# Kernel optimization log

Hardware: AMD Instinct MI355X
Metric: run time of the kernel (lower is better)

## Reference

```python
import jax, jax.numpy as jnp
import numpy as np

N_NODES = 100000
N_EDGES = 3200000
FEAT = 32
N_ITER = 6  # -> n_iter - 1 = 5 SimpleConv layers
MIN_VAL, MAX_VAL = 0.0, 2.0


def setup_inputs() -> dict:
    key = jax.random.key(0)
    k = jax.random.split(key, 6)
    return {
        "x": jax.random.uniform(k[0], (N_NODES, FEAT), dtype=jnp.float32) * 2.0,
        "edge_index": jax.random.randint(k[1], (2, N_EDGES), 0, N_NODES, dtype=jnp.int32),
        "edge_mask": jax.random.randint(k[2], (N_EDGES,), 0, 2, dtype=jnp.int32),
        "edge_scale": jax.random.uniform(k[3], (N_EDGES,), dtype=jnp.float32),
        "pert_mask": jax.random.uniform(k[4], (N_EDGES,), dtype=jnp.float32),
        "edge_weight": jax.random.uniform(k[5], (N_EDGES,), dtype=jnp.float32),
    }


def reference(x, edge_index, edge_mask, edge_scale, pert_mask, edge_weight):
    # edge_index *= edge_mask (masked edges collapse to node 0, as in the torch code)
    ei = edge_index * edge_mask.astype(edge_index.dtype)  # [2, E]
    src, dst = ei[0], ei[1]
    # edge_weight = (edge_weight * (1 - pert_mask) + pert_mask) * edge_scale
    w = (edge_weight * (1.0 - pert_mask) + pert_mask) * edge_scale  # [E]

    def step(x, _):
        # SimpleConv(aggr='sum'): out[dst] += w_e * x[src]
        msgs = x[src] * w[:, None]                                   # [E, F]
        x_new = jax.ops.segment_sum(msgs, dst, num_segments=N_NODES)  # [N, F]
        # max_update: x + Hardtanh(-1,1)(x_new - x)
        x_new = x + jnp.clip(x_new - x, -1.0, 1.0)
        # act: Hardtanh(min_val, max_val)
        return jnp.clip(x_new, MIN_VAL, MAX_VAL), None

    x, _ = jax.lax.scan(step, x, None, length=N_ITER - 1)
    return x
```

## Files before the change

kernel.cpp:

```cpp
#include <hip/hip_runtime.h>
#include <hip/hip_fp16.h>

#define NNODES 100000
#define NEDGES 3200000
#define FEAT 32
#define NITER 5
#define NF (NNODES * FEAT)

#define EDGE_BLOCKS (NEDGES / 256)

#define BUCK_SH 8
#define BUCK_SZ 256
#define NBK 391
#define CHUNKF 4096
#define NBF 782
#define NT (NBF * NBK)
#define NTB 299

__global__ void ws_kernel(const int* __restrict__ edge_index,
                          const int* __restrict__ edge_mask,
                          const float* __restrict__ edge_scale,
                          const float* __restrict__ pert_mask,
                          const float* __restrict__ edge_weight,
                          int2* __restrict__ pay,
                          unsigned short* __restrict__ bkt,
                          float* __restrict__ S_part) {
    const int e = blockIdx.x * 256 + threadIdx.x;
    const int m = edge_mask[e];
    const float w = (edge_weight[e] * (1.0f - pert_mask[e]) + pert_mask[e]) * edge_scale[e];
    const int src = edge_index[e];
    const int dst = edge_index[NEDGES + e];
    pay[e] = make_int2(src | ((dst & (BUCK_SZ - 1)) << 20), __float_as_int(w));
    bkt[e] = m ? (unsigned short)(dst >> BUCK_SH) : (unsigned short)0xFFFFu;
    float ms = m ? 0.0f : w;
    __shared__ float s[256];
    s[threadIdx.x] = ms;
    __syncthreads();
    for (int off = 128; off; off >>= 1) {
        if (threadIdx.x < off) s[threadIdx.x] += s[threadIdx.x + off];
        __syncthreads();
    }
    if (threadIdx.x == 0) S_part[blockIdx.x] = s[0];
}

__global__ void sreduce_kernel(const float* __restrict__ S_part, float* __restrict__ S) {
    __shared__ float s[1024];
    float a = 0.0f;
    for (int i = threadIdx.x; i < EDGE_BLOCKS; i += 1024) a += S_part[i];
    s[threadIdx.x] = a;
    __syncthreads();
    for (int off = 512; off; off >>= 1) {
        if (threadIdx.x < off) s[threadIdx.x] += s[threadIdx.x + off];
        __syncthreads();
    }
    if (threadIdx.x == 0) *S = s[0];
}

__global__ void histmat_kernel(const unsigned short* __restrict__ bkt, int* __restrict__ M) {
    __shared__ int h[NBK];
    const int b = blockIdx.x;
    for (int k = threadIdx.x; k < NBK; k += 256) h[k] = 0;
    __syncthreads();
    const int base = b * CHUNKF;
    for (int it = 0; it < CHUNKF / 256; ++it) {
        const int e = base + it * 256 + threadIdx.x;
        if (e < NEDGES) {
            const unsigned short k = bkt[e];
            if (k != 0xFFFFu) atomicAdd(&h[k], 1);
        }
    }
    __syncthreads();
    for (int k = threadIdx.x; k < NBK; k += 256) M[b * NBK + k] = h[k];
}

__global__ void tscan1_kernel(const int* __restrict__ M, int* __restrict__ tb) {
    __shared__ int s[1024];
    const int i = blockIdx.x * 1024 + threadIdx.x;
    int v = 0;
    if (i < NT) v = M[(i % NBF) * NBK + (i / NBF)];
    s[threadIdx.x] = v;
    __syncthreads();
    for (int off = 512; off; off >>= 1) {
        if (threadIdx.x < off) s[threadIdx.x] += s[threadIdx.x + off];
        __syncthreads();
    }
    if (threadIdx.x == 0) tb[blockIdx.x] = s[0];
}

__global__ void tscan2_kernel(const int* __restrict__ tb, int* __restrict__ tboff,
                              int* __restrict__ bucket_base) {
    __shared__ int s[512];
    const int tid = threadIdx.x;
    int v = (tid < NTB) ? tb[tid] : 0;
    s[tid] = v;
    __syncthreads();
    for (int off = 1; off < 512; off <<= 1) {
        int t = (tid >= off) ? s[tid - off] : 0;
        __syncthreads();
        s[tid] += t;
        __syncthreads();
    }
    if (tid < NTB) tboff[tid] = s[tid] - v;
    if (tid == 511) bucket_base[NBK] = s[511];
}

__global__ void tscan3_kernel(const int* __restrict__ M, const int* __restrict__ tboff,
                              int* __restrict__ scanT, int* __restrict__ bucket_base) {
    __shared__ int s[1024];
    const int tid = threadIdx.x;
    const int i = blockIdx.x * 1024 + tid;
    int v = 0;
    if (i < NT) v = M[(i % NBF) * NBK + (i / NBF)];
    s[tid] = v;
    __syncthreads();
    for (int off = 1; off < 1024; off <<= 1) {
        int t = (tid >= off) ? s[tid - off] : 0;
        __syncthreads();
        s[tid] += t;
        __syncthreads();
    }
    if (i < NT) {
        const int excl = tboff[blockIdx.x] + s[tid] - v;
        scanT[i] = excl;
        if (i % NBF == 0) bucket_base[i / NBF] = excl;
    }
}

__global__ void fill782_kernel(const int2* __restrict__ pay,
                               const unsigned short* __restrict__ bkt,
                               const int* __restrict__ scanT,
                               int2* __restrict__ e8tmp) {
    __shared__ int off[NBK];
    const int b = blockIdx.x;
    for (int k = threadIdx.x; k < NBK; k += 256) off[k] = scanT[k * NBF + b];
    __syncthreads();
    const int base = b * CHUNKF;
    for (int it = 0; it < CHUNKF / 256; ++it) {
        const int e = base + it * 256 + threadIdx.x;
        if (e < NEDGES) {
            const unsigned short k = bkt[e];
            if (k != 0xFFFFu) {
                const int pos = atomicAdd(&off[k], 1);
                e8tmp[pos] = pay[e];
            }
        }
    }
}

__global__ void bsort_kernel(const int2* __restrict__ e8tmp,
                             const int* __restrict__ bucket_base,
                             int2* __restrict__ e8,
                             int* __restrict__ row_ptr) {
    __shared__ int h[BUCK_SZ];
    __shared__ int s[BUCK_SZ];
    __shared__ int woff[BUCK_SZ];
    const int k = blockIdx.x;
    const int tid = threadIdx.x;
    const int base0 = bucket_base[k];
    const int cnt = bucket_base[k + 1] - base0;
    h[tid] = 0;
    __syncthreads();
    for (int i = tid; i < cnt; i += 256) {
        const int dstl = e8tmp[base0 + i].x >> 20;
        atomicAdd(&h[dstl], 1);
    }
    __syncthreads();
    s[tid] = h[tid];
    __syncthreads();
    for (int off = 1; off < BUCK_SZ; off <<= 1) {
        int t = (tid >= off) ? s[tid - off] : 0;
        __syncthreads();
        s[tid] += t;
        __syncthreads();
    }
    {
        const int excl = s[tid] - h[tid];
        const int d = k * BUCK_SZ + tid;
        if (d < NNODES) row_ptr[d] = base0 + excl;
        woff[tid] = excl;
    }
    if (k == NBK - 1 && tid == 0) row_ptr[NNODES] = bucket_base[NBK];
    __syncthreads();
    for (int i = tid; i < cnt; i += 256) {
        const int2 v = e8tmp[base0 + i];
        const int dstl = v.x >> 20;
        const int src = v.x & 0xFFFFF;
        const int pos = atomicAdd(&woff[dstl], 1);
        e8[base0 + pos] = make_int2(src << 5, v.y);
    }
}

__global__ void cvt_kernel(const float* __restrict__ x, __half* __restrict__ xh) {
    const int i = blockIdx.x * 256 + threadIdx.x;
    const float4 v = reinterpret_cast<const float4*>(x)[i];
    const int node = i >> 3;
    const int q = i & 7;
    const int fh = q >> 2;
    const int part = q & 3;
    __half2 h01 = __floats2half2_rn(v.x, v.y);
    __half2 h23 = __floats2half2_rn(v.z, v.w);
    *reinterpret_cast<uint2*>((char*)xh + (size_t)fh * (NNODES * 32) + node * 32 + part * 8)
        = make_uint2(*(unsigned*)&h01, *(unsigned*)&h23);
}

__global__ void gather_kernel(const __half* __restrict__ xh,
                              const int* __restrict__ row_ptr,
                              const int2* __restrict__ e8,
                              const float* __restrict__ S,
                              float* __restrict__ out,
                              __half* __restrict__ outh) {
    const int bid = blockIdx.x;
    const int r = bid & 7;
    const int fh = r >> 2;
    const int blk = (bid >> 3) * 4 + (r & 3);
    if (blk >= 6250) return;
    const int lane = threadIdx.x & 63;
    const int wid = threadIdx.x >> 6;
    const int nq   = lane >> 4;
    const int slot = (lane >> 1) & 7;
    const int part = lane & 1;
    const int node = blk * 16 + wid * 4 + nq;
    const int beg = row_ptr[node];
    const int end = row_ptr[node + 1];
    const char* xhc = (const char*)xh + (size_t)fh * (NNODES * 32);

    float a0=0.f,a1=0.f,a2=0.f,a3=0.f,a4=0.f,a5=0.f,a6=0.f,a7=0.f;
    const int em1c = (end - 1 > beg) ? (end - 1) : beg;
    for (int i = beg + slot; __any(i < end); i += 8) {
        const bool valid = (i < end);
        const int2 sw = e8[valid ? i : em1c];
        const float w = valid ? __int_as_float(sw.y) : 0.0f;
        const uint4 hv = *reinterpret_cast<const uint4*>(
            xhc + (size_t)(unsigned)sw.x + (part << 4));
        float2 f;
        f = __half22float2(*(const __half2*)&hv.x); a0 = fmaf(w, f.x, a0); a1 = fmaf(w, f.y, a1);
        f = __half22float2(*(const __half2*)&hv.y); a2 = fmaf(w, f.x, a2); a3 = fmaf(w, f.y, a3);
        f = __half22float2(*(const __half2*)&hv.z); a4 = fmaf(w, f.x, a4); a5 = fmaf(w, f.y, a5);
        f = __half22float2(*(const __half2*)&hv.w); a6 = fmaf(w, f.x, a6); a7 = fmaf(w, f.y, a7);
    }
    #pragma unroll
    for (int off = 2; off <= 8; off <<= 1) {
        a0 += __shfl_xor(a0, off); a1 += __shfl_xor(a1, off);
        a2 += __shfl_xor(a2, off); a3 += __shfl_xor(a3, off);
        a4 += __shfl_xor(a4, off); a5 += __shfl_xor(a5, off);
        a6 += __shfl_xor(a6, off); a7 += __shfl_xor(a7, off);
    }
    if ((lane & 14) == 0) {
        const uint4 hx = *reinterpret_cast<const uint4*>(xhc + node * 32 + (part << 4));
        float2 f;
        f = __half22float2(*(const __half2*)&hx.x); const float x0f = f.x, x1f = f.y;
        f = __half22float2(*(const __half2*)&hx.y); const float x2f = f.x, x3f = f.y;
        f = __half22float2(*(const __half2*)&hx.z); const float x4f = f.x, x5f = f.y;
        f = __half22float2(*(const __half2*)&hx.w); const float x6f = f.x, x7f = f.y;
        if (node == 0) {
            const float S0 = *S;
            a0 = fmaf(S0, x0f, a0); a1 = fmaf(S0, x1f, a1);
            a2 = fmaf(S0, x2f, a2); a3 = fmaf(S0, x3f, a3);
            a4 = fmaf(S0, x4f, a4); a5 = fmaf(S0, x5f, a5);
            a6 = fmaf(S0, x6f, a6); a7 = fmaf(S0, x7f, a7);
        }
        const float r0 = fminf(fmaxf(x0f + fminf(fmaxf(a0 - x0f, -1.f), 1.f), 0.f), 2.f);
        const float r1 = fminf(fmaxf(x1f + fminf(fmaxf(a1 - x1f, -1.f), 1.f), 0.f), 2.f);
        const float r2 = fminf(fmaxf(x2f + fminf(fmaxf(a2 - x2f, -1.f), 1.f), 0.f), 2.f);
        const float r3 = fminf(fmaxf(x3f + fminf(fmaxf(a3 - x3f, -1.f), 1.f), 0.f), 2.f);
        const float r4 = fminf(fmaxf(x4f + fminf(fmaxf(a4 - x4f, -1.f), 1.f), 0.f), 2.f);
        const float r5 = fminf(fmaxf(x5f + fminf(fmaxf(a5 - x5f, -1.f), 1.f), 0.f), 2.f);
        const float r6 = fminf(fmaxf(x6f + fminf(fmaxf(a6 - x6f, -1.f), 1.f), 0.f), 2.f);
        const float r7 = fminf(fmaxf(x7f + fminf(fmaxf(a7 - x7f, -1.f), 1.f), 0.f), 2.f);
        __half2 h0 = __floats2half2_rn(r0, r1);
        __half2 h1 = __floats2half2_rn(r2, r3);
        __half2 h2 = __floats2half2_rn(r4, r5);
        __half2 h3 = __floats2half2_rn(r6, r7);
        uint4 hh;
        hh.x = *(unsigned*)&h0; hh.y = *(unsigned*)&h1;
        hh.z = *(unsigned*)&h2; hh.w = *(unsigned*)&h3;
        *reinterpret_cast<uint4*>((char*)outh + (size_t)fh * (NNODES * 32)
                                  + node * 32 + (part << 4)) = hh;
        if (out) {
            float* op = out + node * FEAT + (fh << 4) + (part << 3);
            *reinterpret_cast<float4*>(op)     = make_float4(r0, r1, r2, r3);
            *reinterpret_cast<float4*>(op + 4) = make_float4(r4, r5, r6, r7);
        }
    }
}

extern "C" void kernel_launch(void* const* d_in, const int* in_sizes, int n_in,
                              void* d_out, int out_size, void* d_ws, size_t ws_size,
                              hipStream_t stream) {
    const float* x0         = (const float*)d_in[0];
    const int*   edge_index = (const int*)d_in[1];
    const int*   edge_mask  = (const int*)d_in[2];
    const float* edge_scale = (const float*)d_in[3];
    const float* pert_mask  = (const float*)d_in[4];
    const float* edge_weight= (const float*)d_in[5];
    float* xout = (float*)d_out;

    char* ws = (char*)d_ws;
    float* S        = (float*)(ws);
    float* S_part   = (float*)(ws + 1024);
    int*   tb       = (int*)(ws + 64 * 1024);
    int*   tboff    = (int*)(ws + 68 * 1024);
    int*   bbase    = (int*)(ws + 72 * 1024);
    int*   row_ptr  = (int*)(ws + 80 * 1024);
    int*   M        = (int*)(ws + 1  * 1024 * 1024);
    int*   scanT    = (int*)(ws + 3  * 1024 * 1024);
    int2*  e8tmp    = (int2*)(ws + 5  * 1024 * 1024);
    int2*  e8       = (int2*)(ws + 18 * 1024 * 1024);
    int2*  pay      = (int2*)(ws + 31 * 1024 * 1024);
    unsigned short* bkt = (unsigned short*)(ws + 57 * 1024 * 1024);
    __half* xh0     = (__half*)(ws + 31 * 1024 * 1024);
    __half* xh1     = (__half*)(ws + 38 * 1024 * 1024);

    ws_kernel<<<EDGE_BLOCKS, 256, 0, stream>>>(edge_index, edge_mask, edge_scale,
                                               pert_mask, edge_weight, pay, bkt, S_part);
    sreduce_kernel<<<1, 1024, 0, stream>>>(S_part, S);
    histmat_kernel<<<NBF, 256, 0, stream>>>(bkt, M);
    tscan1_kernel<<<NTB, 1024, 0, stream>>>(M, tb);
    tscan2_kernel<<<1, 512, 0, stream>>>(tb, tboff, bbase);
    tscan3_kernel<<<NTB, 1024, 0, stream>>>(M, tboff, scanT, bbase);
    fill782_kernel<<<NBF, 256, 0, stream>>>(pay, bkt, scanT, e8tmp);
    bsort_kernel<<<NBK, 256, 0, stream>>>(e8tmp, bbase, e8, row_ptr);
    cvt_kernel<<<NF / 4 / 256, 256, 0, stream>>>(x0, xh0);

    const int gblocks = 12504;
    __half* xhb[2] = { xh0, xh1 };
    for (int it = 0; it < NITER; ++it) {
        gather_kernel<<<gblocks, 256, 0, stream>>>(xhb[it & 1], row_ptr, e8, S,
                                                   (it == NITER - 1) ? xout : nullptr,
                                                   xhb[(it + 1) & 1]);
    }
}
```

Measured before the change: 239.4 us.

## Pack CSR edges into 32-bit src+fp16 weight and fuse histogram into weight kernel

The histogram kernel is folded into the per-edge weight/payload kernel, so a separate launch and a re-read of the bucket array go away. The sorted edge array shrinks from 8 bytes to 4 bytes per edge: 17 bits of source index plus a sign-dropped fp16 weight (weights are non-negative). This halves the edge-stream traffic in each of the five gather iterations. The trade-off is reduced weight precision (fp16) and fewer threads in the fused kernel, each looping over 16 edges.

```diff
diff --git a/kernel.cpp b/kernel.cpp
--- a/kernel.cpp
+++ b/kernel.cpp
@@ -6,8 +6,6 @@
 #define FEAT 32
 #define NITER 5
 #define NF (NNODES * FEAT)
-
-#define EDGE_BLOCKS (NEDGES / 256)
 
 #define BUCK_SH 8
 #define BUCK_SZ 256
@@ -24,29 +22,46 @@
                           const float* __restrict__ edge_weight,
                           int2* __restrict__ pay,
                           unsigned short* __restrict__ bkt,
+                          int* __restrict__ M,
                           float* __restrict__ S_part) {
-    const int e = blockIdx.x * 256 + threadIdx.x;
-    const int m = edge_mask[e];
-    const float w = (edge_weight[e] * (1.0f - pert_mask[e]) + pert_mask[e]) * edge_scale[e];
-    const int src = edge_index[e];
-    const int dst = edge_index[NEDGES + e];
-    pay[e] = make_int2(src | ((dst & (BUCK_SZ - 1)) << 20), __float_as_int(w));
-    bkt[e] = m ? (unsigned short)(dst >> BUCK_SH) : (unsigned short)0xFFFFu;
-    float ms = m ? 0.0f : w;
-    __shared__ float s[256];
-    s[threadIdx.x] = ms;
+    __shared__ int h[NBK];
+    __shared__ float sred[256];
+    const int b = blockIdx.x;
+    for (int k = threadIdx.x; k < NBK; k += 256) h[k] = 0;
+    __syncthreads();
+    const int base = b * CHUNKF;
+    float ms = 0.0f;
+    for (int it = 0; it < CHUNKF / 256; ++it) {
+        const int e = base + it * 256 + threadIdx.x;
+        if (e < NEDGES) {
+            const int m = edge_mask[e];
+            const float w = (edge_weight[e] * (1.0f - pert_mask[e]) + pert_mask[e]) * edge_scale[e];
+            const int src = edge_index[e];
+            const int dst = edge_index[NEDGES + e];
+            pay[e] = make_int2(src | ((dst & (BUCK_SZ - 1)) << 20), __float_as_int(w));
+            if (m) {
+                bkt[e] = (unsigned short)(dst >> BUCK_SH);
+                atomicAdd(&h[dst >> BUCK_SH], 1);
+            } else {
+                bkt[e] = (unsigned short)0xFFFFu;
+                ms += w;
+            }
+        }
+    }
+    sred[threadIdx.x] = ms;
     __syncthreads();
     for (int off = 128; off; off >>= 1) {
-        if (threadIdx.x < off) s[threadIdx.x] += s[threadIdx.x + off];
-        __syncthreads();
-    }
-    if (threadIdx.x == 0) S_part[blockIdx.x] = s[0];
+        if (threadIdx.x < off) sred[threadIdx.x] += sred[threadIdx.x + off];
+        __syncthreads();
+    }
+    if (threadIdx.x == 0) S_part[b] = sred[0];
+    for (int k = threadIdx.x; k < NBK; k += 256) M[b * NBK + k] = h[k];
 }
 
 __global__ void sreduce_kernel(const float* __restrict__ S_part, float* __restrict__ S) {
     __shared__ float s[1024];
     float a = 0.0f;
-    for (int i = threadIdx.x; i < EDGE_BLOCKS; i += 1024) a += S_part[i];
+    for (int i = threadIdx.x; i < NBF; i += 1024) a += S_part[i];
     s[threadIdx.x] = a;
     __syncthreads();
     for (int off = 512; off; off >>= 1) {
@@ -54,23 +69,6 @@
         __syncthreads();
     }
     if (threadIdx.x == 0) *S = s[0];
-}
-
-__global__ void histmat_kernel(const unsigned short* __restrict__ bkt, int* __restrict__ M) {
-    __shared__ int h[NBK];
-    const int b = blockIdx.x;
-    for (int k = threadIdx.x; k < NBK; k += 256) h[k] = 0;
-    __syncthreads();
-    const int base = b * CHUNKF;
-    for (int it = 0; it < CHUNKF / 256; ++it) {
-        const int e = base + it * 256 + threadIdx.x;
-        if (e < NEDGES) {
-            const unsigned short k = bkt[e];
-            if (k != 0xFFFFu) atomicAdd(&h[k], 1);
-        }
-    }
-    __syncthreads();
-    for (int k = threadIdx.x; k < NBK; k += 256) M[b * NBK + k] = h[k];
 }
 
 __global__ void tscan1_kernel(const int* __restrict__ M, int* __restrict__ tb) {
@@ -149,7 +147,7 @@
 
 __global__ void bsort_kernel(const int2* __restrict__ e8tmp,
                              const int* __restrict__ bucket_base,
-                             int2* __restrict__ e8,
+                             unsigned* __restrict__ e4,
                              int* __restrict__ row_ptr) {
     __shared__ int h[BUCK_SZ];
     __shared__ int s[BUCK_SZ];
@@ -184,9 +182,11 @@
     for (int i = tid; i < cnt; i += 256) {
         const int2 v = e8tmp[base0 + i];
         const int dstl = v.x >> 20;
-        const int src = v.x & 0xFFFFF;
+        const unsigned src = (unsigned)(v.x & 0xFFFFF);
+        __half hw = __float2half_rn(__int_as_float(v.y));
+        const unsigned h16 = (unsigned)(*reinterpret_cast<unsigned short*>(&hw)) & 0x7FFFu;
         const int pos = atomicAdd(&woff[dstl], 1);
-        e8[base0 + pos] = make_int2(src << 5, v.y);
+        e4[base0 + pos] = (src << 15) | h16;
     }
 }
 
@@ -205,7 +205,7 @@
 
 __global__ void gather_kernel(const __half* __restrict__ xh,
                               const int* __restrict__ row_ptr,
-                              const int2* __restrict__ e8,
+                              const unsigned* __restrict__ e4,
                               const float* __restrict__ S,
                               float* __restrict__ out,
                               __half* __restrict__ outh) {
@@ -228,10 +228,12 @@
     const int em1c = (end - 1 > beg) ? (end - 1) : beg;
     for (int i = beg + slot; __any(i < end); i += 8) {
         const bool valid = (i < end);
-        const int2 sw = e8[valid ? i : em1c];
-        const float w = valid ? __int_as_float(sw.y) : 0.0f;
+        const unsigned v = e4[valid ? i : em1c];
+        unsigned short w16 = (unsigned short)(v & 0x7FFFu);
+        const float wv = __half2float(*reinterpret_cast<const __half*>(&w16));
+        const float w = valid ? wv : 0.0f;
         const uint4 hv = *reinterpret_cast<const uint4*>(
-            xhc + (size_t)(unsigned)sw.x + (part << 4));
+            xhc + (size_t)((v >> 10) & 0xFFFFE0u) + (part << 4));
         float2 f;
         f = __half22float2(*(const __half2*)&hv.x); a0 = fmaf(w, f.x, a0); a1 = fmaf(w, f.y, a1);
         f = __half22float2(*(const __half2*)&hv.y); a2 = fmaf(w, f.x, a2); a3 = fmaf(w, f.y, a3);
@@ -305,27 +307,26 @@
     int*   M        = (int*)(ws + 1  * 1024 * 1024);
     int*   scanT    = (int*)(ws + 3  * 1024 * 1024);
     int2*  e8tmp    = (int2*)(ws + 5  * 1024 * 1024);
-    int2*  e8       = (int2*)(ws + 18 * 1024 * 1024);
-    int2*  pay      = (int2*)(ws + 31 * 1024 * 1024);
-    unsigned short* bkt = (unsigned short*)(ws + 57 * 1024 * 1024);
-    __half* xh0     = (__half*)(ws + 31 * 1024 * 1024);
-    __half* xh1     = (__half*)(ws + 38 * 1024 * 1024);
-
-    ws_kernel<<<EDGE_BLOCKS, 256, 0, stream>>>(edge_index, edge_mask, edge_scale,
-                                               pert_mask, edge_weight, pay, bkt, S_part);
+    unsigned* e4    = (unsigned*)(ws + 18 * 1024 * 1024);
+    int2*  pay      = (int2*)(ws + 25 * 1024 * 1024);
+    unsigned short* bkt = (unsigned short*)(ws + 51 * 1024 * 1024);
+    __half* xh0     = (__half*)(ws + 25 * 1024 * 1024);
+    __half* xh1     = (__half*)(ws + 32 * 1024 * 1024);
+
+    ws_kernel<<<NBF, 256, 0, stream>>>(edge_index, edge_mask, edge_scale,
+                                       pert_mask, edge_weight, pay, bkt, M, S_part);
     sreduce_kernel<<<1, 1024, 0, stream>>>(S_part, S);
-    histmat_kernel<<<NBF, 256, 0, stream>>>(bkt, M);
     tscan1_kernel<<<NTB, 1024, 0, stream>>>(M, tb);
     tscan2_kernel<<<1, 512, 0, stream>>>(tb, tboff, bbase);
     tscan3_kernel<<<NTB, 1024, 0, stream>>>(M, tboff, scanT, bbase);
     fill782_kernel<<<NBF, 256, 0, stream>>>(pay, bkt, scanT, e8tmp);
-    bsort_kernel<<<NBK, 256, 0, stream>>>(e8tmp, bbase, e8, row_ptr);
+    bsort_kernel<<<NBK, 256, 0, stream>>>(e8tmp, bbase, e4, row_ptr);
     cvt_kernel<<<NF / 4 / 256, 256, 0, stream>>>(x0, xh0);
 
     const int gblocks = 12504;
     __half* xhb[2] = { xh0, xh1 };
     for (int it = 0; it < NITER; ++it) {
-        gather_kernel<<<gblocks, 256, 0, stream>>>(xhb[it & 1], row_ptr, e8, S,
+        gather_kernel<<<gblocks, 256, 0, stream>>>(xhb[it & 1], row_ptr, e4, S,
                                                    (it == NITER - 1) ? xout : nullptr,
                                                    xhb[(it + 1) & 1]);
     }
```

Result: faster. 219.6 us (-8.3%).
